# Kernel optimization log

Measured on AMD Instinct MI355X. Metric: run time of the kernel, lower is better.

## Reference

```python
import jax, jax.numpy as jnp
import numpy as np


def setup_inputs() -> dict:
    key = jax.random.key(0)
    k1, k2, k3 = jax.random.split(key, 3)
    B, Cin, H, W = 16, 128, 56, 56
    Cout, Kh, Kw = 256, 3, 3
    tensor = jax.random.normal(k1, (B, Cin, H, W), dtype=jnp.float32)
    weights = jax.random.normal(k2, (Cout, Cin, Kh, Kw), dtype=jnp.float32) * 0.05
    bias = jax.random.normal(k3, (Cout,), dtype=jnp.float32) * 0.05
    return {"tensor": tensor, "weights": weights, "bias": bias}


def reference(tensor, weights, bias):
    # OpticalConvolution: unfold (im2col) -> per-output-channel augmented dot
    # products (w . patch + b). Mathematically this is a standard 2D conv with
    # bias, expressed here as one fused conv instead of a per-channel loop.
    stride, padding, dilation = (1, 1), ((1, 1), (1, 1)), (1, 1)
    out = jax.lax.conv_general_dilated(
        tensor, weights,
        window_strides=stride,
        padding=padding,
        rhs_dilation=dilation,
        dimension_numbers=("NCHW", "OIHW", "NCHW"),
    )
    return out + bias[None, :, None, None]  # [B, Cout, H_out, W_out]
```

## Files before the change

kernel.cpp:

```cpp
#include <hip/hip_runtime.h>
#include <hip/hip_bf16.h>

typedef unsigned short ushort_t;
typedef unsigned int uint_t;

#define CIN   128
#define COUT  256
#define HH    56
#define WW    56
#define HWSZ  3136
#define BATCH 16
#define NPIX  50176
#define KTOT  1152

#define PROW_U 68
#define PATCH_U (4 * 58 * 68)

typedef __attribute__((ext_vector_type(8))) short bf16x8;
typedef __attribute__((ext_vector_type(4))) float f32x4;

__device__ __forceinline__ ushort_t f2bf(float v) {
    union { float f; uint_t u; } c; c.f = v;
    uint_t u = c.u;
    u += 0x7FFFu + ((u >> 16) & 1u);
    return (ushort_t)(u >> 16);
}

__device__ __forceinline__ uint_t pk2bf(float lo, float hi) {
    __hip_bfloat162 h = __float22bfloat162_rn(make_float2(lo, hi));
    union { __hip_bfloat162 h; uint_t u; } c; c.h = h;
    return c.u;
}

__global__ __launch_bounds__(256) void wprep(
    const float* __restrict__ weights, ushort_t* __restrict__ A2)
{
    __shared__ ushort_t lds_s[KTOT];
    const int tid = threadIdx.x;
    const int co  = blockIdx.x;
    const float* src = weights + (size_t)co * KTOT;
    #pragma unroll
    for (int k = 0; k < 5; ++k) {
        int idx = tid + k * 256;
        if (idx < KTOT) {
            int ci  = idx / 9;
            int pos = idx - ci * 9;
            lds_s[pos * 128 + ci] = f2bf(src[idx]);
        }
    }
    __syncthreads();
    int mt  = co >> 6;
    int ii  = (co >> 4) & 3;
    int l16 = co & 15;
    if (tid < 144) {
        int s    = tid >> 2;
        int quad = tid & 3;
        uint4 v = *(const uint4*)&lds_s[(s >> 2) * 128 + (s & 3) * 32 + quad * 8];
        *(uint4*)(A2 + ((size_t)((mt * 36 + s) * 4 + ii) * 64 + quad * 16 + l16) * 8) = v;
    }
}

__global__ __launch_bounds__(256, 2) void conv_direct(
    const ushort_t* __restrict__ A2,
    const float* __restrict__ tensor,
    const float* __restrict__ bias,
    float* __restrict__ out)
{
    __shared__ __align__(16) uint_t patch[PATCH_U];
    const int tid  = threadIdx.x;
    const int wave = tid >> 6;
    const int lane = tid & 63;
    const int quad = lane >> 4;
    const int l16  = lane & 15;

    const int bn = blockIdx.x;
    const int b  = bn / 28;
    const int y0 = (bn - b * 28) * 2;

    const uint4 z4 = make_uint4(0u, 0u, 0u, 0u);
    for (int t = tid; t < 204; t += 256) {
        int cell = t / 17, part = t - cell * 17;
        int pr = cell >> 1, xc = (cell & 1) * 57;
        *(uint4*)&patch[(pr * 58 + xc) * PROW_U + part * 4] = z4;
    }
    if (y0 == 0) {
        for (int t = tid; t < 986; t += 256) {
            int cell = t / 17, part = t - cell * 17;
            *(uint4*)&patch[cell * PROW_U + part * 4] = z4;
        }
    }
    if (y0 == 54) {
        for (int t = tid; t < 986; t += 256) {
            int cell = t / 17, part = t - cell * 17;
            *(uint4*)&patch[(3 * 58 + cell) * PROW_U + part * 4] = z4;
        }
    }

    const float* src_b = tensor + (size_t)b * CIN * HWSZ;
    #pragma unroll
    for (int it = 0; it < 16; ++it) {
        int xq = tid & 15;
        int t2 = it * 16 + (tid >> 4);
        int cp = t2 & 63;
        int pr = t2 >> 6;
        int y  = y0 - 1 + pr;
        if (xq < 14 && (uint_t)y < (uint_t)HH) {
            const float* s0 = src_b + (size_t)(2 * cp) * HWSZ + y * WW + xq * 4;
            float4 va = *(const float4*)s0;
            float4 vb = *(const float4*)(s0 + HWSZ);
            uint_t* dst = &patch[(pr * 58 + xq * 4 + 1) * PROW_U + cp];
            dst[0 * PROW_U] = pk2bf(va.x, vb.x);
            dst[1 * PROW_U] = pk2bf(va.y, vb.y);
            dst[2 * PROW_U] = pk2bf(va.z, vb.z);
            dst[3 * PROW_U] = pk2bf(va.w, vb.w);
        }
    }
    __syncthreads();

    const ushort_t* patch_s = (const ushort_t*)patch;
    const ushort_t* bptr[7];
    #pragma unroll
    for (int j = 0; j < 7; ++j) {
        int p  = j * 16 + l16;
        int ro = p / 56;
        int x  = p - ro * 56;
        bptr[j] = patch_s + (ro * 58 + x) * 136 + quad * 8;
    }

    const ushort_t* aBase = A2 + ((size_t)(wave * 144) * 64 + lane) * 8;

    const f32x4 zero = {0.f, 0.f, 0.f, 0.f};
    f32x4 acc[4][7];
    #pragma unroll
    for (int i = 0; i < 4; ++i)
        #pragma unroll
        for (int j = 0; j < 7; ++j) acc[i][j] = zero;

    bf16x8 aCur[4], aNxt[4], bCur[7], bNxt[7];
    #pragma unroll
    for (int i = 0; i < 4; ++i) aCur[i] = *(const bf16x8*)(aBase + i * 512);
    #pragma unroll
    for (int j = 0; j < 7; ++j) bCur[j] = *(const bf16x8*)(bptr[j]);

    #pragma unroll
    for (int s = 0; s < 36; ++s) {
        if (s < 35) {
            const int s1   = s + 1;
            const int pos1 = s1 >> 2;
            const int cc1  = s1 & 3;
            const int off1 = ((pos1 / 3) * 58 + (pos1 % 3)) * 136 + cc1 * 32;
            #pragma unroll
            for (int i = 0; i < 4; ++i)
                aNxt[i] = *(const bf16x8*)(aBase + (size_t)(s1 * 4 + i) * 512);
            #pragma unroll
            for (int j = 0; j < 7; ++j)
                bNxt[j] = *(const bf16x8*)(bptr[j] + off1);
        }
        #pragma unroll
        for (int i = 0; i < 4; ++i)
            #pragma unroll
            for (int j = 0; j < 7; ++j)
                acc[i][j] = __builtin_amdgcn_mfma_f32_16x16x32_bf16(
                    aCur[i], bCur[j], acc[i][j], 0, 0, 0);
        #pragma unroll
        for (int i = 0; i < 4; ++i) aCur[i] = aNxt[i];
        #pragma unroll
        for (int j = 0; j < 7; ++j) bCur[j] = bNxt[j];
    }

    int opix[7];
    #pragma unroll
    for (int j = 0; j < 7; ++j) {
        int p  = j * 16 + l16;
        int ro = p / 56;
        int x  = p - ro * 56;
        opix[j] = (y0 + ro) * WW + x;
    }
    const size_t bout = (size_t)b * (COUT * HWSZ);
    #pragma unroll
    for (int i = 0; i < 4; ++i) {
        #pragma unroll
        for (int r = 0; r < 4; ++r) {
            int co = wave * 64 + i * 16 + quad * 4 + r;
            float bv = bias[co];
            size_t obase = bout + (size_t)co * HWSZ;
            #pragma unroll
            for (int j = 0; j < 7; ++j)
                out[obase + opix[j]] = acc[i][j][r] + bv;
        }
    }
}

__global__ void naive_conv(const float* __restrict__ in, const float* __restrict__ w,
                           const float* __restrict__ bias, float* __restrict__ out, int total) {
    int idx = blockIdx.x * 256 + threadIdx.x;
    if (idx >= total) return;
    int x = idx % WW; int t = idx / WW;
    int y = t % HH; t /= HH;
    int co = t % COUT; int b = t / COUT;
    float s = bias[co];
    const float* wr = w + (size_t)co * KTOT;
    for (int ci = 0; ci < CIN; ++ci) {
        const float* ir = in + (size_t)(b * CIN + ci) * HWSZ;
        for (int kh = 0; kh < 3; ++kh) {
            int yy = y + kh - 1;
            if ((uint_t)yy >= (uint_t)HH) continue;
            for (int kw = 0; kw < 3; ++kw) {
                int xx = x + kw - 1;
                if ((uint_t)xx >= (uint_t)WW) continue;
                s += ir[yy * WW + xx] * wr[ci * 9 + kh * 3 + kw];
            }
        }
    }
    out[idx] = s;
}

extern "C" void kernel_launch(void* const* d_in, const int* in_sizes, int n_in,
                              void* d_out, int out_size, void* d_ws, size_t ws_size,
                              hipStream_t stream) {
    const float* tensor  = (const float*)d_in[0];
    const float* weights = (const float*)d_in[1];
    const float* bias    = (const float*)d_in[2];
    float* out = (float*)d_out;

    const size_t A2_BYTES = (size_t)COUT * KTOT * 2;

    if (ws_size >= A2_BYTES) {
        ushort_t* A2 = (ushort_t*)d_ws;
        wprep<<<COUT, 256, 0, stream>>>(weights, A2);
        conv_direct<<<NPIX / 112, 256, 0, stream>>>(A2, tensor, bias, out);
    } else {
        int total = BATCH * COUT * HWSZ;
        naive_conv<<<(total + 255) / 256, 256, 0, stream>>>(tensor, weights, bias, out, total);
    }
}
```

Before: 111.2 us.

## Tile conv by single output row per block to cut LDS and raise occupancy

Each block now computes one output row (56 pixels, padded to 64 as four 16-wide MFMA tiles) instead of two rows (112 pixels, seven tiles). This shrinks the input patch in LDS from four rows to three and the accumulator set from 28 to 16 tiles, so launch bounds can ask for three blocks per CU. B-operand prefetch from LDS is dropped in favour of direct per-step loads. The cost is more input-row reloading per output (three rows loaded for every one computed instead of four for two) and wasted MFMA work on the padded columns 56..63.

Result: slower. 132.4 us (+19.1%).

```diff
diff --git a/kernel.cpp b/kernel.cpp
--- a/kernel.cpp
+++ b/kernel.cpp
@@ -13,8 +13,8 @@
 #define NPIX  50176
 #define KTOT  1152
 
-#define PROW_U 68
-#define PATCH_U (4 * 58 * 68)
+#define PROW_U  68
+#define PATCH_U ((3 * 58 + 9) * 68)
 
 typedef __attribute__((ext_vector_type(8))) short bf16x8;
 typedef __attribute__((ext_vector_type(4))) float f32x4;
@@ -60,7 +60,7 @@
     }
 }
 
-__global__ __launch_bounds__(256, 2) void conv_direct(
+__global__ __launch_bounds__(256, 3) void conv_direct(
     const ushort_t* __restrict__ A2,
     const float* __restrict__ tensor,
     const float* __restrict__ bias,
@@ -74,41 +74,41 @@
     const int l16  = lane & 15;
 
     const int bn = blockIdx.x;
-    const int b  = bn / 28;
-    const int y0 = (bn - b * 28) * 2;
+    const int b  = bn / 56;
+    const int y0 = bn - b * 56;
 
     const uint4 z4 = make_uint4(0u, 0u, 0u, 0u);
-    for (int t = tid; t < 204; t += 256) {
-        int cell = t / 17, part = t - cell * 17;
-        int pr = cell >> 1, xc = (cell & 1) * 57;
-        *(uint4*)&patch[(pr * 58 + xc) * PROW_U + part * 4] = z4;
+    if (tid < 102) {
+        int cell = tid / 17, part = tid - cell * 17;
+        int sl = cell >> 1, xc = (cell & 1) * 57;
+        *(uint4*)&patch[(sl * 58 + xc) * PROW_U + part * 4] = z4;
     }
     if (y0 == 0) {
-        for (int t = tid; t < 986; t += 256) {
+        for (int t = tid; t < 952; t += 256) {
             int cell = t / 17, part = t - cell * 17;
-            *(uint4*)&patch[cell * PROW_U + part * 4] = z4;
-        }
-    }
-    if (y0 == 54) {
-        for (int t = tid; t < 986; t += 256) {
+            *(uint4*)&patch[(cell + 1) * PROW_U + part * 4] = z4;
+        }
+    }
+    if (y0 == 55) {
+        for (int t = tid; t < 952; t += 256) {
             int cell = t / 17, part = t - cell * 17;
-            *(uint4*)&patch[(3 * 58 + cell) * PROW_U + part * 4] = z4;
+            *(uint4*)&patch[(2 * 58 + cell + 1) * PROW_U + part * 4] = z4;
         }
     }
 
     const float* src_b = tensor + (size_t)b * CIN * HWSZ;
-    #pragma unroll
-    for (int it = 0; it < 16; ++it) {
-        int xq = tid & 15;
-        int t2 = it * 16 + (tid >> 4);
-        int cp = t2 & 63;
-        int pr = t2 >> 6;
-        int y  = y0 - 1 + pr;
+    for (int it = 0; it < 12; ++it) {
+        int t  = it * 256 + tid;
+        int r  = t >> 10;
+        int u  = t & 1023;
+        int cp = u >> 4;
+        int xq = u & 15;
+        int y  = y0 - 1 + r;
         if (xq < 14 && (uint_t)y < (uint_t)HH) {
             const float* s0 = src_b + (size_t)(2 * cp) * HWSZ + y * WW + xq * 4;
             float4 va = *(const float4*)s0;
             float4 vb = *(const float4*)(s0 + HWSZ);
-            uint_t* dst = &patch[(pr * 58 + xq * 4 + 1) * PROW_U + cp];
+            uint_t* dst = &patch[(r * 58 + xq * 4 + 1) * PROW_U + cp];
             dst[0 * PROW_U] = pk2bf(va.x, vb.x);
             dst[1 * PROW_U] = pk2bf(va.y, vb.y);
             dst[2 * PROW_U] = pk2bf(va.z, vb.z);
@@ -118,75 +118,57 @@
     __syncthreads();
 
     const ushort_t* patch_s = (const ushort_t*)patch;
-    const ushort_t* bptr[7];
-    #pragma unroll
-    for (int j = 0; j < 7; ++j) {
-        int p  = j * 16 + l16;
-        int ro = p / 56;
-        int x  = p - ro * 56;
-        bptr[j] = patch_s + (ro * 58 + x) * 136 + quad * 8;
-    }
-
+    const int bbase = l16 * 136 + quad * 8;
     const ushort_t* aBase = A2 + ((size_t)(wave * 144) * 64 + lane) * 8;
 
     const f32x4 zero = {0.f, 0.f, 0.f, 0.f};
-    f32x4 acc[4][7];
+    f32x4 acc[4][4];
     #pragma unroll
     for (int i = 0; i < 4; ++i)
         #pragma unroll
-        for (int j = 0; j < 7; ++j) acc[i][j] = zero;
-
-    bf16x8 aCur[4], aNxt[4], bCur[7], bNxt[7];
+        for (int j = 0; j < 4; ++j) acc[i][j] = zero;
+
+    bf16x8 aCur[4], aNxt[4];
     #pragma unroll
     for (int i = 0; i < 4; ++i) aCur[i] = *(const bf16x8*)(aBase + i * 512);
-    #pragma unroll
-    for (int j = 0; j < 7; ++j) bCur[j] = *(const bf16x8*)(bptr[j]);
 
     #pragma unroll
     for (int s = 0; s < 36; ++s) {
         if (s < 35) {
-            const int s1   = s + 1;
-            const int pos1 = s1 >> 2;
-            const int cc1  = s1 & 3;
-            const int off1 = ((pos1 / 3) * 58 + (pos1 % 3)) * 136 + cc1 * 32;
             #pragma unroll
             for (int i = 0; i < 4; ++i)
-                aNxt[i] = *(const bf16x8*)(aBase + (size_t)(s1 * 4 + i) * 512);
-            #pragma unroll
-            for (int j = 0; j < 7; ++j)
-                bNxt[j] = *(const bf16x8*)(bptr[j] + off1);
-        }
+                aNxt[i] = *(const bf16x8*)(aBase + (size_t)((s + 1) * 4 + i) * 512);
+        }
+        const int pos = s >> 2;
+        const int cc  = s & 3;
+        const int off = ((pos / 3) * 58 + (pos % 3)) * 136 + cc * 32;
         #pragma unroll
-        for (int i = 0; i < 4; ++i)
-            #pragma unroll
-            for (int j = 0; j < 7; ++j)
+        for (int j = 0; j < 4; ++j) {
+            bf16x8 bf = *(const bf16x8*)&patch_s[bbase + j * 2176 + off];
+            #pragma unroll
+            for (int i = 0; i < 4; ++i)
                 acc[i][j] = __builtin_amdgcn_mfma_f32_16x16x32_bf16(
-                    aCur[i], bCur[j], acc[i][j], 0, 0, 0);
-        #pragma unroll
-        for (int i = 0; i < 4; ++i) aCur[i] = aNxt[i];
-        #pragma unroll
-        for (int j = 0; j < 7; ++j) bCur[j] = bNxt[j];
-    }
-
-    int opix[7];
-    #pragma unroll
-    for (int j = 0; j < 7; ++j) {
-        int p  = j * 16 + l16;
-        int ro = p / 56;
-        int x  = p - ro * 56;
-        opix[j] = (y0 + ro) * WW + x;
-    }
-    const size_t bout = (size_t)b * (COUT * HWSZ);
+                    aCur[i], bf, acc[i][j], 0, 0, 0);
+        }
+        if (s < 35) {
+            #pragma unroll
+            for (int i = 0; i < 4; ++i) aCur[i] = aNxt[i];
+        }
+    }
+
+    const size_t rowbase = (size_t)b * (COUT * HWSZ) + y0 * WW;
     #pragma unroll
     for (int i = 0; i < 4; ++i) {
         #pragma unroll
         for (int r = 0; r < 4; ++r) {
             int co = wave * 64 + i * 16 + quad * 4 + r;
             float bv = bias[co];
-            size_t obase = bout + (size_t)co * HWSZ;
-            #pragma unroll
-            for (int j = 0; j < 7; ++j)
-                out[obase + opix[j]] = acc[i][j][r] + bv;
+            size_t obase = rowbase + (size_t)co * HWSZ;
+            #pragma unroll
+            for (int j = 0; j < 3; ++j)
+                out[obase + j * 16 + l16] = acc[i][j][r] + bv;
+            if (l16 < 8)
+                out[obase + 48 + l16] = acc[i][3][r] + bv;
         }
     }
 }
@@ -228,7 +210,7 @@
     if (ws_size >= A2_BYTES) {
         ushort_t* A2 = (ushort_t*)d_ws;
         wprep<<<COUT, 256, 0, stream>>>(weights, A2);
-        conv_direct<<<NPIX / 112, 256, 0, stream>>>(A2, tensor, bias, out);
+        conv_direct<<<BATCH * HH, 256, 0, stream>>>(A2, tensor, bias, out);
     } else {
         int total = BATCH * COUT * HWSZ;
         naive_conv<<<(total + 255) / 256, 256, 0, stream>>>(tensor, weights, bias, out, total);
```

## Re-layout LDS patch into channel-octet slabs and load B fragments just-in-time

Applied to the files above, without the earlier changes.

The shared-memory input patch changes from a pixel-major layout with a padded channel row to a [row][channel-group][x][8 channels] slab layout. Each lane's 16-byte B fragment reads now fall in contiguous per-x chunks, which should change the LDS bank-conflict pattern. Zero-fill of the borders is simplified to match. The double-buffered B register prefetch is removed: each B fragment is loaded from LDS right before its four MFMAs, lowering register pressure but exposing LDS latency unless the compiler schedules around it.

Result: no change. 111.7 us (+0.5%).

```diff
diff --git a/kernel.cpp b/kernel.cpp
--- a/kernel.cpp
+++ b/kernel.cpp
@@ -13,8 +13,10 @@
 #define NPIX  50176
 #define KTOT  1152
 
-#define PROW_U 68
-#define PATCH_U (4 * 58 * 68)
+#define CHX     58
+#define CH_STR  (CHX * 8)
+#define SL_STR  (16 * CH_STR)
+#define PATCH_S (4 * SL_STR)
 
 typedef __attribute__((ext_vector_type(8))) short bf16x8;
 typedef __attribute__((ext_vector_type(4))) float f32x4;
@@ -66,7 +68,8 @@
     const float* __restrict__ bias,
     float* __restrict__ out)
 {
-    __shared__ __align__(16) uint_t patch[PATCH_U];
+    __shared__ __align__(16) ushort_t patch[PATCH_S];
+    uint_t* patch_u = (uint_t*)patch;
     const int tid  = threadIdx.x;
     const int wave = tid >> 6;
     const int lane = tid & 63;
@@ -78,22 +81,18 @@
     const int y0 = (bn - b * 28) * 2;
 
     const uint4 z4 = make_uint4(0u, 0u, 0u, 0u);
-    for (int t = tid; t < 204; t += 256) {
-        int cell = t / 17, part = t - cell * 17;
-        int pr = cell >> 1, xc = (cell & 1) * 57;
-        *(uint4*)&patch[(pr * 58 + xc) * PROW_U + part * 4] = z4;
+    if (tid < 128) {
+        int sc = tid >> 1;
+        int xc = (tid & 1) * 57;
+        *(uint4*)&patch_u[(sc * CHX + xc) * 4] = z4;
     }
     if (y0 == 0) {
-        for (int t = tid; t < 986; t += 256) {
-            int cell = t / 17, part = t - cell * 17;
-            *(uint4*)&patch[cell * PROW_U + part * 4] = z4;
-        }
+        for (int t = tid; t < 928; t += 256)
+            *(uint4*)&patch_u[t * 4] = z4;
     }
     if (y0 == 54) {
-        for (int t = tid; t < 986; t += 256) {
-            int cell = t / 17, part = t - cell * 17;
-            *(uint4*)&patch[(3 * 58 + cell) * PROW_U + part * 4] = z4;
-        }
+        for (int t = tid; t < 928; t += 256)
+            *(uint4*)&patch_u[(3 * 16 * CHX + t) * 4] = z4;
     }
 
     const float* src_b = tensor + (size_t)b * CIN * HWSZ;
@@ -108,23 +107,22 @@
             const float* s0 = src_b + (size_t)(2 * cp) * HWSZ + y * WW + xq * 4;
             float4 va = *(const float4*)s0;
             float4 vb = *(const float4*)(s0 + HWSZ);
-            uint_t* dst = &patch[(pr * 58 + xq * 4 + 1) * PROW_U + cp];
-            dst[0 * PROW_U] = pk2bf(va.x, vb.x);
-            dst[1 * PROW_U] = pk2bf(va.y, vb.y);
-            dst[2 * PROW_U] = pk2bf(va.z, vb.z);
-            dst[3 * PROW_U] = pk2bf(va.w, vb.w);
+            uint_t* dst = &patch_u[((pr * 16 + (cp >> 2)) * CHX + xq * 4 + 1) * 4 + (cp & 3)];
+            dst[0 * 4] = pk2bf(va.x, vb.x);
+            dst[1 * 4] = pk2bf(va.y, vb.y);
+            dst[2 * 4] = pk2bf(va.z, vb.z);
+            dst[3 * 4] = pk2bf(va.w, vb.w);
         }
     }
     __syncthreads();
 
-    const ushort_t* patch_s = (const ushort_t*)patch;
-    const ushort_t* bptr[7];
+    int bbase[7];
     #pragma unroll
     for (int j = 0; j < 7; ++j) {
         int p  = j * 16 + l16;
         int ro = p / 56;
         int x  = p - ro * 56;
-        bptr[j] = patch_s + (ro * 58 + x) * 136 + quad * 8;
+        bbase[j] = ro * SL_STR + quad * CH_STR + x * 8;
     }
 
     const ushort_t* aBase = A2 + ((size_t)(wave * 144) * 64 + lane) * 8;
@@ -136,36 +134,32 @@
         #pragma unroll
         for (int j = 0; j < 7; ++j) acc[i][j] = zero;
 
-    bf16x8 aCur[4], aNxt[4], bCur[7], bNxt[7];
+    bf16x8 aCur[4], aNxt[4];
     #pragma unroll
     for (int i = 0; i < 4; ++i) aCur[i] = *(const bf16x8*)(aBase + i * 512);
-    #pragma unroll
-    for (int j = 0; j < 7; ++j) bCur[j] = *(const bf16x8*)(bptr[j]);
 
     #pragma unroll
     for (int s = 0; s < 36; ++s) {
         if (s < 35) {
-            const int s1   = s + 1;
-            const int pos1 = s1 >> 2;
-            const int cc1  = s1 & 3;
-            const int off1 = ((pos1 / 3) * 58 + (pos1 % 3)) * 136 + cc1 * 32;
             #pragma unroll
             for (int i = 0; i < 4; ++i)
-                aNxt[i] = *(const bf16x8*)(aBase + (size_t)(s1 * 4 + i) * 512);
-            #pragma unroll
-            for (int j = 0; j < 7; ++j)
-                bNxt[j] = *(const bf16x8*)(bptr[j] + off1);
-        }
+                aNxt[i] = *(const bf16x8*)(aBase + (size_t)((s + 1) * 4 + i) * 512);
+        }
+        const int pos = s >> 2;
+        const int cc  = s & 3;
+        const int off = (pos / 3) * SL_STR + cc * 4 * CH_STR + (pos % 3) * 8;
         #pragma unroll
-        for (int i = 0; i < 4; ++i)
-            #pragma unroll
-            for (int j = 0; j < 7; ++j)
+        for (int j = 0; j < 7; ++j) {
+            bf16x8 bf = *(const bf16x8*)&patch[bbase[j] + off];
+            #pragma unroll
+            for (int i = 0; i < 4; ++i)
                 acc[i][j] = __builtin_amdgcn_mfma_f32_16x16x32_bf16(
-                    aCur[i], bCur[j], acc[i][j], 0, 0, 0);
-        #pragma unroll
-        for (int i = 0; i < 4; ++i) aCur[i] = aNxt[i];
-        #pragma unroll
-        for (int j = 0; j < 7; ++j) bCur[j] = bNxt[j];
+                    aCur[i], bf, acc[i][j], 0, 0, 0);
+        }
+        if (s < 35) {
+            #pragma unroll
+            for (int i = 0; i < 4; ++i) aCur[i] = aNxt[i];
+        }
     }
 
     int opix[7];
```
